# Kernel optimization log

Hardware: AMD Instinct MI355X
Metric: run time of the kernel (lower is better)

The kernel has to match this reference:

```python
import jax, jax.numpy as jnp
import numpy as np
from jax.scipy.linalg import expm, solve_triangular

B, N, K, A, V = 2, 256, 16, 16, 32000
ALPHA = 1.0
LAMBDA_BELIEF = 1.0
EPS = 1e-8   # kl_divergence jitter
EPS2 = 1e-6  # pairwise-KL jitter


def _spd(key, b, n, k, scale=0.3):
    a = jax.random.normal(key, (b, n, k, k)) * scale
    return jnp.einsum('bnkl,bnml->bnkm', a, a) + jnp.eye(k)


def setup_inputs() -> dict:
    key = jax.random.key(0)
    ks = jax.random.split(key, 9)
    mu = jax.random.normal(ks[0], (B, N, K))
    Sigma = _spd(ks[1], B, N, K)
    phi = jax.random.normal(ks[2], (B, N, A)) * 0.05
    mu_prior = jax.random.normal(ks[3], (B, N, K))
    Sigma_prior = _spd(ks[4], B, N, K)
    beta = jax.random.uniform(ks[5], (B, N, N)) / N
    W_out = jax.random.normal(ks[6], (V, K)) * 0.02
    R = jax.random.normal(ks[7], (A, K, K))
    generators = (R - jnp.swapaxes(R, -1, -2)) * 0.1  # skew-symmetric Lie generators
    targets = jax.random.randint(ks[8], (B, N), 0, V)
    return {"mu": mu, "Sigma": Sigma, "phi": phi, "mu_prior": mu_prior,
            "Sigma_prior": Sigma_prior, "beta": beta, "W_out": W_out,
            "generators": generators, "targets": targets}


def _bexpm(M):
    # batched matrix exponential over leading dims
    shape = M.shape
    return jax.vmap(expm)(M.reshape(-1, shape[-2], shape[-1])).reshape(shape)


def _potential(mu, Sigma, phi, mu_prior, Sigma_prior, beta, W_out, generators, targets):
    I = jnp.eye(K, dtype=mu.dtype)

    # --- V_self: alpha * sum_n KL(q_n || p_n), explicit-inverse formulation ---
    Sq = Sigma + EPS * I
    Sp = Sigma_prior + EPS * I
    Sp_inv = jnp.linalg.inv(Sp)
    trace_t = jnp.einsum('bnij,bnji->bn', Sp_inv, Sq)
    dmu = mu_prior - mu
    mahal = jnp.einsum('bni,bnij,bnj->bn', dmu, Sp_inv, dmu)
    logdet = jnp.linalg.slogdet(Sp)[1] - jnp.linalg.slogdet(Sq)[1]
    kl_self = 0.5 * (trace_t + mahal - K + logdet)
    V_self = ALPHA * kl_self.sum(-1)

    # --- V_align: pairwise KL under Lie transport Omega_ij = e^{phi_i G} e^{-phi_j G} ---
    phi_mat = jnp.einsum('bna,aij->bnij', phi, generators)          # (B,N,K,K)
    exp_phi = _bexpm(phi_mat)
    exp_neg_phi = _bexpm(-phi_mat)
    Omega = jnp.einsum('bikl,bjlm->bijkm', exp_phi, exp_neg_phi)    # (B,N,N,K,K)
    mu_t = jnp.einsum('bijkl,bjl->bijk', Omega, mu)                 # (B,N,N,K)
    # Omega Sigma_j Omega^T (congruence -> SPD)
    Sigma_t = jnp.einsum('bijkl,bjlm,bijnm->bijkn', Omega, Sigma, Omega)

    Stp = Sigma_t + EPS2 * I
    L_p = jnp.linalg.cholesky(Stp)                                  # (B,N,N,K,K)
    Sigma_i = jnp.broadcast_to((Sigma + EPS2 * I)[:, :, None], (B, N, N, K, K))
    Y = solve_triangular(L_p, Sigma_i, lower=True)
    Z = solve_triangular(jnp.swapaxes(L_p, -1, -2), Y, lower=False)
    trace_term = jnp.diagonal(Z, axis1=-2, axis2=-1).sum(-1)        # (B,N,N)

    delta = mu_t - mu[:, :, None, :]
    v = solve_triangular(L_p, delta[..., None], lower=True)[..., 0]
    mahal_term = (v ** 2).sum(-1)

    logdet_p = 2.0 * jnp.log(jnp.diagonal(L_p, axis1=-2, axis2=-1) + EPS2).sum(-1)
    L_q = jnp.linalg.cholesky(Sigma + EPS2 * I)                     # (B,N,K,K)
    logdet_q = 2.0 * jnp.log(jnp.diagonal(L_q, axis1=-2, axis2=-1) + EPS2).sum(-1)

    kl_all = 0.5 * (trace_term + mahal_term - K + logdet_p - logdet_q[:, :, None])
    kl_all = jnp.maximum(kl_all, 0.0)
    kl_all = kl_all * (1.0 - jnp.eye(N, dtype=mu.dtype))            # zero diagonal
    V_align = LAMBDA_BELIEF * (beta * kl_all).sum((-2, -1))

    # --- V_ce: cross entropy over W_out projection of mu ---
    logits = jnp.einsum('bnk,vk->bnv', mu, W_out)
    logp = jax.nn.log_softmax(logits, axis=-1)
    ce = -jnp.take_along_axis(logp, targets[..., None], axis=-1)[..., 0]
    V_ce = ce.sum(-1)

    return V_self + V_align + V_ce


def reference(mu, Sigma, phi, mu_prior, Sigma_prior, beta, W_out, generators, targets):
    return _potential(mu, Sigma, phi, mu_prior, Sigma_prior, beta, W_out, generators, targets)
```

## Files before the change

kernel.cpp:

```cpp
#include <hip/hip_runtime.h>
#include <math.h>

#define NB 2
#define NN 256
#define KD 16
#define VV 32000
#define EPS_SELF 1e-8f
#define EPS_AL   1e-6f
#define NNODES (NB*NN)

#define CE_ROWS 8
#define CE_CH   32
#define CE_CHUNK (VV/CE_CH)

#define OFF_MT  0
#define OFF_O   (NNODES*16)
#define OFF_P   (OFF_O + NNODES*256)
#define OFF_LD  (OFF_P + NNODES*256)
#define OFF_KLS (OFF_LD + NNODES)
#define OFF_AP  (OFF_KLS + NNODES)
#define OFF_Y   (OFF_AP + NNODES)
#define OFF_W   (OFF_Y + NNODES*16)
#define OFF_CEP (OFF_W + NNODES)
#define OFF_CNT (OFF_CEP + NNODES*CE_CH)
#define WS_FLOATS (OFF_CNT + 4)

#define WAVE_SYNC() asm volatile("s_waitcnt lgkmcnt(0)" ::: "memory")

__device__ __forceinline__ void ld4(float* dst, const float4 v) {
  dst[0] = v.x; dst[1] = v.y; dst[2] = v.z; dst[3] = v.w;
}

__device__ __forceinline__ float dot16a(const float* a, const float* b) {
  float acc = 0.f;
  #pragma unroll
  for (int j = 0; j < 16; ++j) acc = fmaf(a[j], b[j], acc);
  return acc;
}

__device__ __forceinline__ float dot4(float4 a, float4 b) {
  return fmaf(a.x, b.x, fmaf(a.y, b.y, fmaf(a.z, b.z, a.w * b.w)));
}

__device__ __forceinline__ void gj16(float aq[4], const int g, const int c, float* ldacc) {
  #pragma unroll
  for (int k = 0; k < 16; ++k) {
    float d    = __shfl(aq[k & 3], ((k >> 2) << 4) | k);
    float rowk = __shfl(aq[k & 3], ((k >> 2) << 4) | c);
    float ck[4];
    #pragma unroll
    for (int q = 0; q < 4; ++q) ck[q] = __shfl(aq[q], (g << 4) | k);
    if (ldacc) *ldacc += logf(d);
    float dinv = 1.f / d;
    #pragma unroll
    for (int q = 0; q < 4; ++q) {
      int r = 4*g + q;
      float vgen = fmaf(-ck[q] * dinv, rowk, aq[q]);
      aq[q] = (r == k) ? ((c == k) ? dinv : aq[q] * dinv)
                       : ((c == k) ? (-ck[q] * dinv) : vgen);
    }
  }
}

template<int QUIRK>
__device__ __forceinline__ float ge16_logdet(float aq[4], const int g, const int c) {
  float ld = 0.f;
  #pragma unroll
  for (int k = 0; k < 16; ++k) {
    float d    = __shfl(aq[k & 3], ((k >> 2) << 4) | k);
    float rowk = __shfl(aq[k & 3], ((k >> 2) << 4) | c);
    float ck[4];
    #pragma unroll
    for (int q = 0; q < 4; ++q) ck[q] = __shfl(aq[q], (g << 4) | k);
    ld += QUIRK ? 2.f * logf(sqrtf(d) + EPS_AL) : logf(d);
    float dinv = 1.f / d;
    #pragma unroll
    for (int q = 0; q < 4; ++q) {
      int r = 4*g + q;
      float upd = fmaf(-ck[q] * dinv, rowk, aq[q]);
      aq[q] = (r > k && c > k) ? upd : aq[q];
    }
  }
  return ld;
}

__global__ __launch_bounds__(256, 2) void fusedA_kernel(
    const float* __restrict__ mu, const float* __restrict__ Sigma,
    const float* __restrict__ phi, const float* __restrict__ mu_prior,
    const float* __restrict__ Sigma_prior, const float* __restrict__ gen,
    const float* __restrict__ W, float* __restrict__ ws)
{
  __shared__ __align__(16) float smem[4][980];
  const int tid = threadIdx.x;
  const int bid = blockIdx.x;

  if (bid < 256) {
    if (bid == 0 && tid == 0) *(unsigned*)(ws + OFF_CNT) = 0u;
    const int w = tid >> 6, l = tid & 63;
    const int g = l >> 4, c = l & 15;
    const int unit = bid * 4 + w;
    const int role = unit & 1, node = unit >> 1;
    float* COLp = &smem[w][0];
    float* ROWp = &smem[w][320];
    float* AUXp = &smem[w][640];

    if (role == 0) {
      float phis[16];
      {
        const float4* p4 = (const float4*)(phi + node*16);
        ld4(phis, p4[0]); ld4(phis+4, p4[1]); ld4(phis+8, p4[2]); ld4(phis+12, p4[3]);
      }
      float x[4] = {0.f, 0.f, 0.f, 0.f};
      #pragma unroll
      for (int aa = 0; aa < 16; ++aa) {
        float4 gq = *(const float4*)(gen + aa*256 + c*16 + 4*g);
        x[0] = fmaf(phis[aa], gq.x, x[0]);
        x[1] = fmaf(phis[aa], gq.y, x[1]);
        x[2] = fmaf(phis[aa], gq.z, x[2]);
        x[3] = fmaf(phis[aa], gq.w, x[3]);
      }
      #pragma unroll
      for (int q = 0; q < 4; ++q) x[q] *= -0.125f;

      #pragma unroll
      for (int q = 0; q < 4; ++q) ROWp[(4*g+q)*20 + c] = x[q];
      WAVE_SYNC();
      float Mrow[4][16];
      #pragma unroll
      for (int q = 0; q < 4; ++q)
        #pragma unroll
        for (int j4 = 0; j4 < 4; ++j4)
          ld4(&Mrow[q][4*j4], *(const float4*)&ROWp[(4*g+q)*20 + 4*j4]);

      float t[4];
      #pragma unroll
      for (int q = 0; q < 4; ++q) t[q] = ((4*g+q) == c ? 1.f : 0.f) + x[q]*0.125f;
      for (int k = 7; k >= 1; --k) {
        *(float4*)&COLp[c*20 + 4*g] = make_float4(t[0], t[1], t[2], t[3]);
        WAVE_SYNC();
        float T[16];
        #pragma unroll
        for (int j4 = 0; j4 < 4; ++j4) ld4(&T[4*j4], *(const float4*)&COLp[c*20 + 4*j4]);
        #pragma unroll
        for (int q = 0; q < 4; ++q)
          t[q] = ((4*g+q) == c ? 1.f : 0.f) + dot16a(Mrow[q], T) / (float)k;
      }
      for (int s = 0; s < 3; ++s) {
        *(float4*)&COLp[c*20 + 4*g] = make_float4(t[0], t[1], t[2], t[3]);
        #pragma unroll
        for (int q = 0; q < 4; ++q) ROWp[(4*g+q)*20 + c] = t[q];
        WAVE_SYNC();
        float T[16];
        #pragma unroll
        for (int j4 = 0; j4 < 4; ++j4) ld4(&T[4*j4], *(const float4*)&COLp[c*20 + 4*j4]);
        float nt[4];
        #pragma unroll
        for (int q = 0; q < 4; ++q) {
          float acc = 0.f;
          #pragma unroll
          for (int j4 = 0; j4 < 4; ++j4) {
            float4 rv = *(const float4*)&ROWp[(4*g+q)*20 + 4*j4];
            acc = fmaf(rv.x, T[4*j4+0], acc);
            acc = fmaf(rv.y, T[4*j4+1], acc);
            acc = fmaf(rv.z, T[4*j4+2], acc);
            acc = fmaf(rv.w, T[4*j4+3], acc);
          }
          nt[q] = acc;
        }
        #pragma unroll
        for (int q = 0; q < 4; ++q) t[q] = nt[q];
      }
      *(float4*)&COLp[c*20 + 4*g] = make_float4(t[0], t[1], t[2], t[3]);
      WAVE_SYNC();
      float Ecol[16];
      #pragma unroll
      for (int j4 = 0; j4 < 4; ++j4) ld4(&Ecol[4*j4], *(const float4*)&COLp[c*20 + 4*j4]);

      float w1q[4];
      #pragma unroll
      for (int q = 0; q < 4; ++q) {
        float S[16];
        const float4* s4 = (const float4*)(Sigma + node*256 + (4*g+q)*16);
        ld4(S, s4[0]); ld4(S+4, s4[1]); ld4(S+8, s4[2]); ld4(S+12, s4[3]);
        w1q[q] = dot16a(S, Ecol);
      }
      *(float4*)&AUXp[c*20 + 4*g] = make_float4(w1q[0], w1q[1], w1q[2], w1q[3]);
      WAVE_SYNC();
      float W1c[16];
      #pragma unroll
      for (int j4 = 0; j4 < 4; ++j4) ld4(&W1c[4*j4], *(const float4*)&AUXp[c*20 + 4*j4]);

      float sh[4];
      #pragma unroll
      for (int q = 0; q < 4; ++q) {
        float Er[16];
        #pragma unroll
        for (int j4 = 0; j4 < 4; ++j4) ld4(&Er[4*j4], *(const float4*)&COLp[(4*g+q)*20 + 4*j4]);
        sh[q] = dot16a(Er, W1c) + ((4*g+q) == c ? EPS_AL : 0.f);
      }

      float mtc;
      {
        float muv[16];
        const float4* m4 = (const float4*)(mu + node*16);
        ld4(muv, m4[0]); ld4(muv+4, m4[1]); ld4(muv+8, m4[2]); ld4(muv+12, m4[3]);
        mtc = dot16a(Ecol, muv);
      }
      float mt4[4];
      #pragma unroll
      for (int q = 0; q < 4; ++q) mt4[q] = __shfl(mtc, 4*g + q);

      *(float4*)(ws + OFF_O + node*256 + c*16 + 4*g) =
          make_float4(fmaf(mt4[0], mtc, sh[0]), fmaf(mt4[1], mtc, sh[1]),
                      fmaf(mt4[2], mtc, sh[2]), fmaf(mt4[3], mtc, sh[3]));
      if (g == 0) ws[OFF_MT + node*16 + c] = mtc;

      gj16(sh, g, c, (float*)nullptr);
      *(float4*)(ws + OFF_P + node*256 + c*16 + 4*g) = make_float4(sh[0], sh[1], sh[2], sh[3]);

      float part = sh[0]*mt4[0] + sh[1]*mt4[1] + sh[2]*mt4[2] + sh[3]*mt4[3];
      part += __shfl_xor(part, 16);
      part += __shfl_xor(part, 32);
      if (g == 0) ws[OFF_Y + node*16 + c] = part;
      float wv = mtc * part;
      wv += __shfl_xor(wv, 1); wv += __shfl_xor(wv, 2);
      wv += __shfl_xor(wv, 4); wv += __shfl_xor(wv, 8);
      if (l == 0) ws[OFF_W + node] = wv;
    } else {
      float sp[4];
      {
        float4 v = *(const float4*)(Sigma_prior + node*256 + c*16 + 4*g);
        sp[0] = v.x + ((4*g+0 == c) ? EPS_SELF : 0.f);
        sp[1] = v.y + ((4*g+1 == c) ? EPS_SELF : 0.f);
        sp[2] = v.z + ((4*g+2 == c) ? EPS_SELF : 0.f);
        sp[3] = v.w + ((4*g+3 == c) ? EPS_SELF : 0.f);
      }
      float ldSp = 0.f;
      gj16(sp, g, c, &ldSp);

      float dmur[4], dmuc;
      {
        float4 a = *(const float4*)(mu_prior + node*16 + 4*g);
        float4 b = *(const float4*)(mu + node*16 + 4*g);
        dmur[0] = a.x - b.x; dmur[1] = a.y - b.y; dmur[2] = a.z - b.z; dmur[3] = a.w - b.w;
        dmuc = mu_prior[node*16 + c] - mu[node*16 + c];
      }
      float4 sv = *(const float4*)(Sigma + node*256 + c*16 + 4*g);
      float val = 0.f;
      {
        float s0 = sv.x + ((4*g+0 == c) ? EPS_SELF : 0.f);
        float s1 = sv.y + ((4*g+1 == c) ? EPS_SELF : 0.f);
        float s2 = sv.z + ((4*g+2 == c) ? EPS_SELF : 0.f);
        float s3 = sv.w + ((4*g+3 == c) ? EPS_SELF : 0.f);
        val = fmaf(sp[0], s0 + dmur[0]*dmuc, val);
        val = fmaf(sp[1], s1 + dmur[1]*dmuc, val);
        val = fmaf(sp[2], s2 + dmur[2]*dmuc, val);
        val = fmaf(sp[3], s3 + dmur[3]*dmuc, val);
      }
      #pragma unroll
      for (int o = 32; o; o >>= 1) val += __shfl_xor(val, o);

      float sq[4];
      sq[0] = sv.x + ((4*g+0 == c) ? EPS_SELF : 0.f);
      sq[1] = sv.y + ((4*g+1 == c) ? EPS_SELF : 0.f);
      sq[2] = sv.z + ((4*g+2 == c) ? EPS_SELF : 0.f);
      sq[3] = sv.w + ((4*g+3 == c) ? EPS_SELF : 0.f);
      float ldSq = ge16_logdet<0>(sq, g, c);
      float sg[4];
      sg[0] = sv.x + ((4*g+0 == c) ? EPS_AL : 0.f);
      sg[1] = sv.y + ((4*g+1 == c) ? EPS_AL : 0.f);
      sg[2] = sv.z + ((4*g+2 == c) ? EPS_AL : 0.f);
      sg[3] = sv.w + ((4*g+3 == c) ? EPS_AL : 0.f);
      float ldq = ge16_logdet<1>(sg, g, c);
      if (l == 0) {
        ws[OFF_KLS + node] = 0.5f * (val - 16.f + ldSp - ldSq);
        ws[OFF_LD + node]  = ldq;
      }
    }
  } else {
    const int idx = bid - 256;
    const int grp = idx & 63;
    const int ch  = idx >> 6;
    const int row0 = grp * CE_ROWS;
    float* mu_s = &smem[0][0];
    float* wred = &smem[0][128];

    if (tid < CE_ROWS*16) mu_s[tid] = mu[row0*16 + tid];
    __syncthreads();

    int z = __shfl((int)0, tid);
    const float4* M4 = (const float4*)(mu_s + z);
    float4 Rv[32];
    #pragma unroll
    for (int i = 0; i < 32; ++i) {
      Rv[i] = M4[i];
      asm volatile("" : "+v"(Rv[i].x), "+v"(Rv[i].y), "+v"(Rv[i].z), "+v"(Rv[i].w));
    }

    float acc[CE_ROWS];
    #pragma unroll
    for (int r = 0; r < CE_ROWS; ++r) acc[r] = 0.f;

    const float4* W4 = (const float4*)W;
    const int v0 = ch * CE_CHUNK;
    for (int v = v0 + tid; v < v0 + CE_CHUNK; v += 256) {
      float4 q0 = W4[v*4+0], q1 = W4[v*4+1], q2 = W4[v*4+2], q3 = W4[v*4+3];
      #pragma unroll
      for (int r = 0; r < CE_ROWS; ++r) {
        float lg = dot4(q0, Rv[4*r]) + dot4(q1, Rv[4*r+1])
                 + dot4(q2, Rv[4*r+2]) + dot4(q3, Rv[4*r+3]);
        acc[r] += __expf(lg);
      }
    }
    #pragma unroll
    for (int r = 0; r < CE_ROWS; ++r)
      #pragma unroll
      for (int o = 32; o; o >>= 1) acc[r] += __shfl_xor(acc[r], o);
    const int w = tid >> 6, l = tid & 63;
    if (l == 0) {
      #pragma unroll
      for (int r = 0; r < CE_ROWS; ++r) wred[w*CE_ROWS + r] = acc[r];
    }
    __syncthreads();
    if (tid < CE_ROWS)
      ws[OFF_CEP + (row0 + tid)*CE_CH + ch] =
          wred[tid] + wred[CE_ROWS + tid] + wred[2*CE_ROWS + tid] + wred[3*CE_ROWS + tid];
  }
}

#define PSTR 260
__global__ __launch_bounds__(256) void alignB_kernel(
    const float* __restrict__ beta, const float* __restrict__ mu,
    const float* __restrict__ W, const int* __restrict__ targets,
    float* __restrict__ ws, float* __restrict__ out)
{
  __shared__ __align__(16) float OI[16*PSTR];
  __shared__ __align__(16) float PJ[16*PSTR];
  __shared__ __align__(16) float mtI[256];
  __shared__ __align__(16) float yJ[256];
  __shared__ float wJ[16], ldI[16], ldJ[16], red[4];
  __shared__ int lastflag;
  const int tid = threadIdx.x;
  const int ti = tid & 15, tj = tid >> 4;
  const int bx = blockIdx.x & 15, by = (blockIdx.x >> 4) & 15, bz = blockIdx.x >> 8;
  const int nodeI0 = bz*256 + by*16, nodeJ0 = bz*256 + bx*16;

  for (int idx = tid; idx < 16*256; idx += 256) {
    int row = idx >> 8, col = idx & 255;
    OI[row*PSTR + col] = ws[OFF_O + (nodeI0 + row)*256 + col];
    PJ[row*PSTR + col] = ws[OFF_P + (nodeJ0 + row)*256 + col];
  }
  mtI[tid] = ws[OFF_MT + nodeI0*16 + tid];
  yJ[tid]  = ws[OFF_Y  + nodeJ0*16 + tid];
  if (tid < 16) {
    wJ[tid]  = ws[OFF_W  + nodeJ0 + tid];
    ldI[tid] = ws[OFF_LD + nodeI0 + tid];
    ldJ[tid] = ws[OFF_LD + nodeJ0 + tid];
  }
  __syncthreads();

  const float4* oi4 = (const float4*)&OI[ti*PSTR];
  const float4* pj4 = (const float4*)&PJ[tj*PSTR];
  float tr = 0.f;
  #pragma unroll 16
  for (int t = 0; t < 64; ++t) {
    float4 xv = oi4[t], yv = pj4[t];
    tr = fmaf(xv.x, yv.x, tr);
    tr = fmaf(xv.y, yv.y, tr);
    tr = fmaf(xv.z, yv.z, tr);
    tr = fmaf(xv.w, yv.w, tr);
  }
  const float4* mi4 = (const float4*)&mtI[ti*16];
  const float4* yj4 = (const float4*)&yJ[tj*16];
  float diy = dot4(mi4[0], yj4[0]) + dot4(mi4[1], yj4[1])
            + dot4(mi4[2], yj4[2]) + dot4(mi4[3], yj4[3]);

  float kl = 0.5f * (tr + wJ[tj] - 2.f*diy - 16.f + ldJ[tj] - ldI[ti]);
  kl = fmaxf(kl, 0.f);
  int gi = by*16 + ti, gj = bx*16 + tj;
  float contrib = (gi == gj) ? 0.f : kl * beta[bz*65536 + gi*256 + gj];
  #pragma unroll
  for (int o = 32; o; o >>= 1) contrib += __shfl_down(contrib, o);
  __syncthreads();
  if ((tid & 63) == 0) red[tid >> 6] = contrib;
  __syncthreads();
  if (tid == 0) {
    ws[OFF_AP + (bz*16 + by)*16 + bx] = red[0] + red[1] + red[2] + red[3];
    unsigned old = __hip_atomic_fetch_add((unsigned*)(ws + OFF_CNT), 1u,
                                          __ATOMIC_ACQ_REL, __HIP_MEMORY_SCOPE_AGENT);
    lastflag = (old == 511u);
  }
  __syncthreads();

  if (lastflag) {
    double* dred = (double*)OI;
    double v[2];
    #pragma unroll
    for (int b = 0; b < 2; ++b) {
      int row = b*256 + tid;
      float s = 0.f;
      #pragma unroll
      for (int c2 = 0; c2 < CE_CH; ++c2) s += ws[OFF_CEP + row*CE_CH + c2];
      int t = targets[row];
      float dt = 0.f;
      const float4* wt4 = (const float4*)(W + t*16);
      const float4* mr4 = (const float4*)(mu + row*16);
      #pragma unroll
      for (int j4 = 0; j4 < 4; ++j4) {
        float4 a = mr4[j4], bb = wt4[j4];
        dt = fmaf(a.x, bb.x, dt); dt = fmaf(a.y, bb.y, dt);
        dt = fmaf(a.z, bb.z, dt); dt = fmaf(a.w, bb.w, dt);
      }
      double ce = (double)logf(s) - (double)dt;
      v[b] = (double)ws[OFF_KLS + row] + (double)ws[OFF_AP + row] + ce;
    }
    for (int b = 0; b < 2; ++b) {
      dred[tid] = v[b];
      __syncthreads();
      for (int h = 128; h > 0; h >>= 1) {
        if (tid < h) dred[tid] += dred[tid + h];
        __syncthreads();
      }
      if (tid == 0) out[b] = (float)dred[0];
      __syncthreads();
    }
  }
}

extern "C" void kernel_launch(void* const* d_in, const int* in_sizes, int n_in,
                              void* d_out, int out_size, void* d_ws, size_t ws_size,
                              hipStream_t stream) {
  const float* mu          = (const float*)d_in[0];
  const float* Sigma       = (const float*)d_in[1];
  const float* phi         = (const float*)d_in[2];
  const float* mu_prior    = (const float*)d_in[3];
  const float* Sigma_prior = (const float*)d_in[4];
  const float* beta        = (const float*)d_in[5];
  const float* W_out       = (const float*)d_in[6];
  const float* gen         = (const float*)d_in[7];
  const int*   targets     = (const int*)d_in[8];
  float* out = (float*)d_out;
  float* ws  = (float*)d_ws;
  if (ws_size < (size_t)WS_FLOATS * sizeof(float)) return;

  fusedA_kernel<<<256 + (NNODES/CE_ROWS)*CE_CH, 256, 0, stream>>>(
      mu, Sigma, phi, mu_prior, Sigma_prior, gen, W_out, ws);
  alignB_kernel<<<NB*16*16, 256, 0, stream>>>(beta, mu, W_out, targets, ws, out);
}
```

Measured before the change: 46.23 us.

## Merge prep, CE and pairwise-KL kernels into one persistent grid-synced kernel

Merges the two kernels into a single 512-block launch. The first 256 blocks do per-node prep and then a smaller vocabulary slice, while the other 256 take larger slices. The vocabulary is split unevenly across 8 slots to balance that load. A global atomic counter with a spin-wait stands in for the kernel boundary before the pairwise-KL phase, which removes the second launch and its gap. The risks are deadlock if not all 512 blocks are co-resident, the cost of spinning, and an added memset launch to reset the counters.

```diff
diff --git a/kernel.cpp b/kernel.cpp
--- a/kernel.cpp
+++ b/kernel.cpp
@@ -10,8 +10,9 @@
 #define NNODES (NB*NN)
 
 #define CE_ROWS 8
-#define CE_CH   32
-#define CE_CHUNK (VV/CE_CH)
+#define CE_SLOTS 8
+#define CE_SMALL 2816
+#define CE_LARGE 5184
 
 #define OFF_MT  0
 #define OFF_O   (NNODES*16)
@@ -22,7 +23,7 @@
 #define OFF_Y   (OFF_AP + NNODES)
 #define OFF_W   (OFF_Y + NNODES*16)
 #define OFF_CEP (OFF_W + NNODES)
-#define OFF_CNT (OFF_CEP + NNODES*CE_CH)
+#define OFF_CNT (OFF_CEP + NNODES*CE_SLOTS)
 #define WS_FLOATS (OFF_CNT + 4)
 
 #define WAVE_SYNC() asm volatile("s_waitcnt lgkmcnt(0)" ::: "memory")
@@ -84,25 +85,31 @@
   return ld;
 }
 
-__global__ __launch_bounds__(256, 2) void fusedA_kernel(
+#define PSTR 260
+
+__global__ __launch_bounds__(256, 2) void mega_kernel(
     const float* __restrict__ mu, const float* __restrict__ Sigma,
     const float* __restrict__ phi, const float* __restrict__ mu_prior,
     const float* __restrict__ Sigma_prior, const float* __restrict__ gen,
-    const float* __restrict__ W, float* __restrict__ ws)
+    const float* __restrict__ W, const float* __restrict__ beta,
+    const int* __restrict__ targets, float* __restrict__ ws,
+    float* __restrict__ out)
 {
-  __shared__ __align__(16) float smem[4][980];
+  __shared__ __align__(16) float smem[8896];
+  __shared__ int lastflag;
   const int tid = threadIdx.x;
   const int bid = blockIdx.x;
+  unsigned* prep_cnt  = (unsigned*)(ws + OFF_CNT);
+  unsigned* align_cnt = prep_cnt + 1;
 
   if (bid < 256) {
-    if (bid == 0 && tid == 0) *(unsigned*)(ws + OFF_CNT) = 0u;
     const int w = tid >> 6, l = tid & 63;
     const int g = l >> 4, c = l & 15;
     const int unit = bid * 4 + w;
     const int role = unit & 1, node = unit >> 1;
-    float* COLp = &smem[w][0];
-    float* ROWp = &smem[w][320];
-    float* AUXp = &smem[w][640];
+    float* COLp = &smem[w*980];
+    float* ROWp = COLp + 320;
+    float* AUXp = COLp + 640;
 
     if (role == 0) {
       float phis[16];
@@ -277,13 +284,25 @@
         ws[OFF_LD + node]  = ldq;
       }
     }
-  } else {
-    const int idx = bid - 256;
-    const int grp = idx & 63;
-    const int ch  = idx >> 6;
+    __syncthreads();
+    if (tid == 0)
+      __hip_atomic_fetch_add(prep_cnt, 1u, __ATOMIC_RELEASE, __HIP_MEMORY_SCOPE_AGENT);
+    __syncthreads();
+  }
+
+  {
+    int grp, slot, v0, v1;
+    if (bid < 256) {
+      grp = bid & 63; slot = bid >> 6;
+      v0 = slot * CE_SMALL; v1 = v0 + CE_SMALL;
+    } else {
+      int b = bid - 256;
+      grp = b & 63; int ch = b >> 6; slot = 4 + ch;
+      v0 = 4*CE_SMALL + ch * CE_LARGE; v1 = v0 + CE_LARGE;
+    }
     const int row0 = grp * CE_ROWS;
-    float* mu_s = &smem[0][0];
-    float* wred = &smem[0][128];
+    float* mu_s = smem;
+    float* wred = smem + 128;
 
     if (tid < CE_ROWS*16) mu_s[tid] = mu[row0*16 + tid];
     __syncthreads();
@@ -302,8 +321,7 @@
     for (int r = 0; r < CE_ROWS; ++r) acc[r] = 0.f;
 
     const float4* W4 = (const float4*)W;
-    const int v0 = ch * CE_CHUNK;
-    for (int v = v0 + tid; v < v0 + CE_CHUNK; v += 256) {
+    for (int v = v0 + tid; v < v1; v += 256) {
       float4 q0 = W4[v*4+0], q1 = W4[v*4+1], q2 = W4[v*4+2], q3 = W4[v*4+3];
       #pragma unroll
       for (int r = 0; r < CE_ROWS; ++r) {
@@ -323,84 +341,87 @@
     }
     __syncthreads();
     if (tid < CE_ROWS)
-      ws[OFF_CEP + (row0 + tid)*CE_CH + ch] =
+      ws[OFF_CEP + (row0 + tid)*CE_SLOTS + slot] =
           wred[tid] + wred[CE_ROWS + tid] + wred[2*CE_ROWS + tid] + wred[3*CE_ROWS + tid];
   }
-}
-
-#define PSTR 260
-__global__ __launch_bounds__(256) void alignB_kernel(
-    const float* __restrict__ beta, const float* __restrict__ mu,
-    const float* __restrict__ W, const int* __restrict__ targets,
-    float* __restrict__ ws, float* __restrict__ out)
-{
-  __shared__ __align__(16) float OI[16*PSTR];
-  __shared__ __align__(16) float PJ[16*PSTR];
-  __shared__ __align__(16) float mtI[256];
-  __shared__ __align__(16) float yJ[256];
-  __shared__ float wJ[16], ldI[16], ldJ[16], red[4];
-  __shared__ int lastflag;
-  const int tid = threadIdx.x;
-  const int ti = tid & 15, tj = tid >> 4;
-  const int bx = blockIdx.x & 15, by = (blockIdx.x >> 4) & 15, bz = blockIdx.x >> 8;
-  const int nodeI0 = bz*256 + by*16, nodeJ0 = bz*256 + bx*16;
-
-  for (int idx = tid; idx < 16*256; idx += 256) {
-    int row = idx >> 8, col = idx & 255;
-    OI[row*PSTR + col] = ws[OFF_O + (nodeI0 + row)*256 + col];
-    PJ[row*PSTR + col] = ws[OFF_P + (nodeJ0 + row)*256 + col];
-  }
-  mtI[tid] = ws[OFF_MT + nodeI0*16 + tid];
-  yJ[tid]  = ws[OFF_Y  + nodeJ0*16 + tid];
-  if (tid < 16) {
-    wJ[tid]  = ws[OFF_W  + nodeJ0 + tid];
-    ldI[tid] = ws[OFF_LD + nodeI0 + tid];
-    ldJ[tid] = ws[OFF_LD + nodeJ0 + tid];
-  }
-  __syncthreads();
-
-  const float4* oi4 = (const float4*)&OI[ti*PSTR];
-  const float4* pj4 = (const float4*)&PJ[tj*PSTR];
-  float tr = 0.f;
-  #pragma unroll 16
-  for (int t = 0; t < 64; ++t) {
-    float4 xv = oi4[t], yv = pj4[t];
-    tr = fmaf(xv.x, yv.x, tr);
-    tr = fmaf(xv.y, yv.y, tr);
-    tr = fmaf(xv.z, yv.z, tr);
-    tr = fmaf(xv.w, yv.w, tr);
-  }
-  const float4* mi4 = (const float4*)&mtI[ti*16];
-  const float4* yj4 = (const float4*)&yJ[tj*16];
-  float diy = dot4(mi4[0], yj4[0]) + dot4(mi4[1], yj4[1])
-            + dot4(mi4[2], yj4[2]) + dot4(mi4[3], yj4[3]);
-
-  float kl = 0.5f * (tr + wJ[tj] - 2.f*diy - 16.f + ldJ[tj] - ldI[ti]);
-  kl = fmaxf(kl, 0.f);
-  int gi = by*16 + ti, gj = bx*16 + tj;
-  float contrib = (gi == gj) ? 0.f : kl * beta[bz*65536 + gi*256 + gj];
-  #pragma unroll
-  for (int o = 32; o; o >>= 1) contrib += __shfl_down(contrib, o);
-  __syncthreads();
-  if ((tid & 63) == 0) red[tid >> 6] = contrib;
+
   __syncthreads();
   if (tid == 0) {
-    ws[OFF_AP + (bz*16 + by)*16 + bx] = red[0] + red[1] + red[2] + red[3];
-    unsigned old = __hip_atomic_fetch_add((unsigned*)(ws + OFF_CNT), 1u,
-                                          __ATOMIC_ACQ_REL, __HIP_MEMORY_SCOPE_AGENT);
-    lastflag = (old == 511u);
+    while (__hip_atomic_load(prep_cnt, __ATOMIC_ACQUIRE, __HIP_MEMORY_SCOPE_AGENT) != 256u)
+      __builtin_amdgcn_s_sleep(8);
   }
   __syncthreads();
 
+  {
+    const int ti = tid & 15, tj = tid >> 4;
+    const int bx = bid & 15, by = (bid >> 4) & 15, bz = bid >> 8;
+    const int nodeI0 = bz*256 + by*16, nodeJ0 = bz*256 + bx*16;
+    float* OI  = smem;
+    float* PJ  = smem + 4160;
+    float* mtI = smem + 8320;
+    float* yJ  = smem + 8576;
+    float* wJ  = smem + 8832;
+    float* ldI = smem + 8848;
+    float* ldJ = smem + 8864;
+    float* red = smem + 8880;
+
+    for (int idx = tid; idx < 16*256; idx += 256) {
+      int row = idx >> 8, col = idx & 255;
+      OI[row*PSTR + col] = ws[OFF_O + (nodeI0 + row)*256 + col];
+      PJ[row*PSTR + col] = ws[OFF_P + (nodeJ0 + row)*256 + col];
+    }
+    mtI[tid] = ws[OFF_MT + nodeI0*16 + tid];
+    yJ[tid]  = ws[OFF_Y  + nodeJ0*16 + tid];
+    if (tid < 16) {
+      wJ[tid]  = ws[OFF_W  + nodeJ0 + tid];
+      ldI[tid] = ws[OFF_LD + nodeI0 + tid];
+      ldJ[tid] = ws[OFF_LD + nodeJ0 + tid];
+    }
+    __syncthreads();
+
+    const float4* oi4 = (const float4*)&OI[ti*PSTR];
+    const float4* pj4 = (const float4*)&PJ[tj*PSTR];
+    float tr = 0.f;
+    #pragma unroll 16
+    for (int t = 0; t < 64; ++t) {
+      float4 xv = oi4[t], yv = pj4[t];
+      tr = fmaf(xv.x, yv.x, tr);
+      tr = fmaf(xv.y, yv.y, tr);
+      tr = fmaf(xv.z, yv.z, tr);
+      tr = fmaf(xv.w, yv.w, tr);
+    }
+    const float4* mi4 = (const float4*)&mtI[ti*16];
+    const float4* yj4 = (const float4*)&yJ[tj*16];
+    float diy = dot4(mi4[0], yj4[0]) + dot4(mi4[1], yj4[1])
+              + dot4(mi4[2], yj4[2]) + dot4(mi4[3], yj4[3]);
+
+    float kl = 0.5f * (tr + wJ[tj] - 2.f*diy - 16.f + ldJ[tj] - ldI[ti]);
+    kl = fmaxf(kl, 0.f);
+    int gi = by*16 + ti, gj = bx*16 + tj;
+    float contrib = (gi == gj) ? 0.f : kl * beta[bz*65536 + gi*256 + gj];
+    #pragma unroll
+    for (int o = 32; o; o >>= 1) contrib += __shfl_down(contrib, o);
+    __syncthreads();
+    if ((tid & 63) == 0) red[tid >> 6] = contrib;
+    __syncthreads();
+    if (tid == 0) {
+      ws[OFF_AP + (bz*16 + by)*16 + bx] = red[0] + red[1] + red[2] + red[3];
+      unsigned old = __hip_atomic_fetch_add(align_cnt, 1u,
+                                            __ATOMIC_ACQ_REL, __HIP_MEMORY_SCOPE_AGENT);
+      lastflag = (old == 511u);
+    }
+    __syncthreads();
+  }
+
   if (lastflag) {
-    double* dred = (double*)OI;
+    double* dred = (double*)smem;
     double v[2];
     #pragma unroll
     for (int b = 0; b < 2; ++b) {
       int row = b*256 + tid;
       float s = 0.f;
       #pragma unroll
-      for (int c2 = 0; c2 < CE_CH; ++c2) s += ws[OFF_CEP + row*CE_CH + c2];
+      for (int c2 = 0; c2 < CE_SLOTS; ++c2) s += ws[OFF_CEP + row*CE_SLOTS + c2];
       int t = targets[row];
       float dt = 0.f;
       const float4* wt4 = (const float4*)(W + t*16);
@@ -443,7 +464,7 @@
   float* ws  = (float*)d_ws;
   if (ws_size < (size_t)WS_FLOATS * sizeof(float)) return;
 
-  fusedA_kernel<<<256 + (NNODES/CE_ROWS)*CE_CH, 256, 0, stream>>>(
-      mu, Sigma, phi, mu_prior, Sigma_prior, gen, W_out, ws);
-  alignB_kernel<<<NB*16*16, 256, 0, stream>>>(beta, mu, W_out, targets, ws, out);
-}
+  hipMemsetAsync((void*)(ws + OFF_CNT), 0, 2*sizeof(unsigned), stream);
+  mega_kernel<<<512, 256, 0, stream>>>(mu, Sigma, phi, mu_prior, Sigma_prior,
+                                       gen, W_out, beta, targets, ws, out);
+}
```

Measured after the change: 51.05 us. 1.1x slower.

## Shrink CE row tiles to double block count and vectorize alignment staging loads

Applied to the files above, without the earlier changes.

The cross-entropy partition work is split into 4-row groups instead of 8-row groups, which doubles the number of CE blocks (4096) and halves the registers each one needs. Launch bounds are raised so more waves fit per SIMD. The second kernel now stages the O and P tiles into shared memory with float4 loads instead of scalar ones. The trade-off is that each W_out row is now read by twice as many blocks, raising global/L2 traffic, in exchange for more parallelism and occupancy.

```diff
diff --git a/kernel.cpp b/kernel.cpp
--- a/kernel.cpp
+++ b/kernel.cpp
@@ -9,9 +9,10 @@
 #define EPS_AL   1e-6f
 #define NNODES (NB*NN)
 
-#define CE_ROWS 8
-#define CE_CH   32
-#define CE_CHUNK (VV/CE_CH)
+#define CE_ROWS 4
+#define CE_SLOTS 32
+#define CE_CHUNK 1000
+#define CE_BLOCKS (128*CE_SLOTS)
 
 #define OFF_MT  0
 #define OFF_O   (NNODES*16)
@@ -22,7 +23,7 @@
 #define OFF_Y   (OFF_AP + NNODES)
 #define OFF_W   (OFF_Y + NNODES*16)
 #define OFF_CEP (OFF_W + NNODES)
-#define OFF_CNT (OFF_CEP + NNODES*CE_CH)
+#define OFF_CNT (OFF_CEP + NNODES*CE_SLOTS)
 #define WS_FLOATS (OFF_CNT + 4)
 
 #define WAVE_SYNC() asm volatile("s_waitcnt lgkmcnt(0)" ::: "memory")
@@ -84,7 +85,7 @@
   return ld;
 }
 
-__global__ __launch_bounds__(256, 2) void fusedA_kernel(
+__global__ __launch_bounds__(256, 4) void kernelA(
     const float* __restrict__ mu, const float* __restrict__ Sigma,
     const float* __restrict__ phi, const float* __restrict__ mu_prior,
     const float* __restrict__ Sigma_prior, const float* __restrict__ gen,
@@ -101,8 +102,8 @@
     const int unit = bid * 4 + w;
     const int role = unit & 1, node = unit >> 1;
     float* COLp = &smem[w][0];
-    float* ROWp = &smem[w][320];
-    float* AUXp = &smem[w][640];
+    float* ROWp = COLp + 320;
+    float* AUXp = COLp + 640;
 
     if (role == 0) {
       float phis[16];
@@ -278,21 +279,22 @@
       }
     }
   } else {
-    const int idx = bid - 256;
-    const int grp = idx & 63;
-    const int ch  = idx >> 6;
+    const int idx  = bid - 256;
+    const int grp  = idx & 127;
+    const int slot = idx >> 7;
+    const int v0 = slot * CE_CHUNK, v1 = v0 + CE_CHUNK;
     const int row0 = grp * CE_ROWS;
     float* mu_s = &smem[0][0];
-    float* wred = &smem[0][128];
+    float* wred = &smem[0][64];
 
     if (tid < CE_ROWS*16) mu_s[tid] = mu[row0*16 + tid];
     __syncthreads();
 
     int z = __shfl((int)0, tid);
     const float4* M4 = (const float4*)(mu_s + z);
-    float4 Rv[32];
-    #pragma unroll
-    for (int i = 0; i < 32; ++i) {
+    float4 Rv[16];
+    #pragma unroll
+    for (int i = 0; i < 16; ++i) {
       Rv[i] = M4[i];
       asm volatile("" : "+v"(Rv[i].x), "+v"(Rv[i].y), "+v"(Rv[i].z), "+v"(Rv[i].w));
     }
@@ -302,8 +304,7 @@
     for (int r = 0; r < CE_ROWS; ++r) acc[r] = 0.f;
 
     const float4* W4 = (const float4*)W;
-    const int v0 = ch * CE_CHUNK;
-    for (int v = v0 + tid; v < v0 + CE_CHUNK; v += 256) {
+    for (int v = v0 + tid; v < v1; v += 256) {
       float4 q0 = W4[v*4+0], q1 = W4[v*4+1], q2 = W4[v*4+2], q3 = W4[v*4+3];
       #pragma unroll
       for (int r = 0; r < CE_ROWS; ++r) {
@@ -323,13 +324,13 @@
     }
     __syncthreads();
     if (tid < CE_ROWS)
-      ws[OFF_CEP + (row0 + tid)*CE_CH + ch] =
+      ws[OFF_CEP + (row0 + tid)*CE_SLOTS + slot] =
           wred[tid] + wred[CE_ROWS + tid] + wred[2*CE_ROWS + tid] + wred[3*CE_ROWS + tid];
   }
 }
 
 #define PSTR 260
-__global__ __launch_bounds__(256) void alignB_kernel(
+__global__ __launch_bounds__(256, 2) void kernelB(
     const float* __restrict__ beta, const float* __restrict__ mu,
     const float* __restrict__ W, const int* __restrict__ targets,
     float* __restrict__ ws, float* __restrict__ out)
@@ -345,10 +346,17 @@
   const int bx = blockIdx.x & 15, by = (blockIdx.x >> 4) & 15, bz = blockIdx.x >> 8;
   const int nodeI0 = bz*256 + by*16, nodeJ0 = bz*256 + bx*16;
 
-  for (int idx = tid; idx < 16*256; idx += 256) {
-    int row = idx >> 8, col = idx & 255;
-    OI[row*PSTR + col] = ws[OFF_O + (nodeI0 + row)*256 + col];
-    PJ[row*PSTR + col] = ws[OFF_P + (nodeJ0 + row)*256 + col];
+  {
+    const float4* src_o = (const float4*)(ws + OFF_O + nodeI0*256);
+    const float4* src_p = (const float4*)(ws + OFF_P + nodeJ0*256);
+    float4* dst_o = (float4*)OI;
+    float4* dst_p = (float4*)PJ;
+    #pragma unroll
+    for (int q = tid; q < 1024; q += 256) {
+      int row = q >> 6, c4 = q & 63;
+      dst_o[row*65 + c4] = src_o[q];
+      dst_p[row*65 + c4] = src_p[q];
+    }
   }
   mtI[tid] = ws[OFF_MT + nodeI0*16 + tid];
   yJ[tid]  = ws[OFF_Y  + nodeJ0*16 + tid];
@@ -400,7 +408,7 @@
       int row = b*256 + tid;
       float s = 0.f;
       #pragma unroll
-      for (int c2 = 0; c2 < CE_CH; ++c2) s += ws[OFF_CEP + row*CE_CH + c2];
+      for (int c2 = 0; c2 < CE_SLOTS; ++c2) s += ws[OFF_CEP + row*CE_SLOTS + c2];
       int t = targets[row];
       float dt = 0.f;
       const float4* wt4 = (const float4*)(W + t*16);
@@ -443,7 +451,7 @@
   float* ws  = (float*)d_ws;
   if (ws_size < (size_t)WS_FLOATS * sizeof(float)) return;
 
-  fusedA_kernel<<<256 + (NNODES/CE_ROWS)*CE_CH, 256, 0, stream>>>(
+  kernelA<<<256 + CE_BLOCKS, 256, 0, stream>>>(
       mu, Sigma, phi, mu_prior, Sigma_prior, gen, W_out, ws);
-  alignB_kernel<<<NB*16*16, 256, 0, stream>>>(beta, mu, W_out, targets, ws, out);
-}
+  kernelB<<<NB*16*16, 256, 0, stream>>>(beta, mu, W_out, targets, ws, out);
+}
```

After: 46.11 us. Within noise of the previous version (-0.2%).
